# Kernel optimization log

Hardware: AMD Instinct MI355X
Metric: run time of the kernel (lower is better)

The kernel has to match this reference:

```python
import jax, jax.numpy as jnp
import numpy as np
from jax import lax

B, K, C, P = 16, 4096, 256, 1024
NSAMPLE = 16
RADIUS = 0.3
NUM_CLASS, NUMD = 18, 1
OUT_CH = 3 + NUMD + NUM_CLASS  # 22
EPS = 1e-5


def fps(xyz, npoint):
    # furthest point sampling; xyz (B,N,3) -> (B,npoint) int32
    b, n, _ = xyz.shape
    def body(carry, _):
        mind, last = carry
        lx = jnp.take_along_axis(xyz, last[:, None, None], axis=1)  # (B,1,3)
        d = jnp.sum((xyz - lx) ** 2, -1)
        mind = jnp.minimum(mind, d)
        nxt = jnp.argmax(mind, -1).astype(jnp.int32)
        return (mind, nxt), nxt
    i0 = jnp.zeros((b,), jnp.int32)
    _, rest = lax.scan(body, (jnp.full((b, n), 1e10, xyz.dtype), i0), None, length=npoint - 1)
    return jnp.concatenate([i0[None], rest], 0).T  # (B,npoint)


def ball_query(xyz, new_xyz, radius, nsample):
    # first `nsample` points (in index order) within radius; pad with first hit
    k = xyz.shape[1]
    d2 = jnp.sum((new_xyz[:, :, None, :] - xyz[:, None, :, :]) ** 2, -1)  # (B,P,K)
    keyi = jnp.where(d2 < radius * radius, jnp.arange(k, dtype=jnp.int32), k)
    idx = jnp.sort(keyi, axis=-1)[..., :nsample]  # (B,P,S)
    first = idx[..., :1]
    idx = jnp.where(idx >= k, first, idx)
    return jnp.clip(idx, 0, k - 1)


def bn(x, g, b, axes):
    # BatchNorm (training-mode batch statistics), channel on last axis
    m = jnp.mean(x, axes, keepdims=True)
    v = jnp.var(x, axes, keepdims=True)
    return (x - m) * lax.rsqrt(v + EPS) * g + b


def setup_inputs() -> dict:
    key = jax.random.key(0)
    ks = jax.random.split(key, 24)
    s = 0.02
    inp = {
        'xyz': jax.random.normal(ks[0], (B, K, 3), jnp.float32),
        'features': jax.random.normal(ks[1], (B, C, K), jnp.float32),
        # shared MLP (Conv2d 1x1, no bias, followed by BN2d)
        'mlp_w0': jax.random.normal(ks[2], (128, C + 3), jnp.float32) * s,
        'mlp_g0': jnp.ones((128,), jnp.float32), 'mlp_be0': jnp.zeros((128,), jnp.float32),
        'mlp_w1': jax.random.normal(ks[3], (128, 128), jnp.float32) * s,
        'mlp_g1': jnp.ones((128,), jnp.float32), 'mlp_be1': jnp.zeros((128,), jnp.float32),
        'mlp_w2': jax.random.normal(ks[4], (128, 128), jnp.float32) * s,
        'mlp_g2': jnp.ones((128,), jnp.float32), 'mlp_be2': jnp.zeros((128,), jnp.float32),
        # head: conv1d(128,128)+bn, conv1d(128,128)+bn, conv1d(128,22)
        'w1': jax.random.normal(ks[5], (128, 128), jnp.float32) * s, 'b1': jnp.zeros((128,), jnp.float32),
        'g1': jnp.ones((128,), jnp.float32), 'be1': jnp.zeros((128,), jnp.float32),
        'w2': jax.random.normal(ks[6], (128, 128), jnp.float32) * s, 'b2': jnp.zeros((128,), jnp.float32),
        'g2': jnp.ones((128,), jnp.float32), 'be2': jnp.zeros((128,), jnp.float32),
        'w3': jax.random.normal(ks[7], (OUT_CH, 128), jnp.float32) * s, 'b3': jnp.zeros((OUT_CH,), jnp.float32),
    }
    return inp


def reference(xyz, features, mlp_w0, mlp_g0, mlp_be0, mlp_w1, mlp_g1, mlp_be1,
              mlp_w2, mlp_g2, mlp_be2, w1, b1, g1, be1, w2, b2, g2, be2, w3, b3):
    # --- vote aggregation: FPS + ball query + grouped shared-MLP + max pool ---
    fps_idx = fps(xyz, P)                                   # (B,P)
    new_xyz = jax.vmap(lambda p, i: p[i])(xyz, fps_idx)      # (B,P,3)
    gidx = ball_query(lax.stop_gradient(xyz), lax.stop_gradient(new_xyz), RADIUS, NSAMPLE)
    gxyz = jax.vmap(lambda p, i: p[i])(xyz, gidx)            # (B,P,S,3)
    gxyz = (gxyz - new_xyz[:, :, None, :]) / RADIUS          # normalize_xyz
    feats_t = jnp.swapaxes(features, 1, 2)                   # (B,K,C)
    gfeat = jax.vmap(lambda f, i: f[i])(feats_t, gidx)       # (B,P,S,C)
    h = jnp.concatenate([gxyz, gfeat], -1)                   # (B,P,S,3+C) use_xyz
    for w, g, b in ((mlp_w0, mlp_g0, mlp_be0), (mlp_w1, mlp_g1, mlp_be1), (mlp_w2, mlp_g2, mlp_be2)):
        h = jax.nn.relu(bn(jnp.einsum('bpsc,oc->bpso', h, w), g, b, (0, 1, 2)))
    agg = jnp.max(h, axis=2)                                 # (B,P,128)
    # --- conv1d + BN + ReLU head ---
    n1 = jax.nn.relu(bn(jnp.einsum('bpc,oc->bpo', agg, w1) + b1, g1, be1, (0, 1)))
    n2 = jax.nn.relu(bn(jnp.einsum('bpc,oc->bpo', n1, w2) + b2, g2, be2, (0, 1)))
    net = jnp.einsum('bpc,oc->bpo', n2, w3) + b3             # (B,P,3+numd+num_class)
    # --- decode_scores (mode='') ---
    center = new_xyz + net[..., :3]
    return jnp.concatenate([center, net[..., 3:]], -1)        # (B,P,22)
```

## Files before the change

kernel.cpp:

```cpp
#include <hip/hip_runtime.h>
#include <math.h>

#define Bsz 16
#define Kpt 4096
#define Cft 256
#define Pnp 1024
#define Smp 16
#define OUTCH 22
#define M0 (Bsz * Pnp * Smp)
#define M1 (Bsz * Pnp)
#define NSLOT 32

#define OFF_FT      ((size_t)0)
#define OFF_YA      ((size_t)8388608)
#define OFF_M2      ((size_t)25165824)
#define OFF_YF1     ((size_t)27262976)
#define OFF_YF2     ((size_t)28311552)
#define OFF_W0T     ((size_t)30408704)
#define OFF_W1T     ((size_t)30425088)
#define OFF_W2T     ((size_t)30433280)
#define OFF_WF1T    ((size_t)30441472)
#define OFF_WF2T    ((size_t)30449664)
#define OFF_STATS   ((size_t)30457856)
#define OFF_GIDX    ((size_t)30498816)
#define OFF_NEWXYZ  ((size_t)30760960)

#define ST_STRIDE (NSLOT * 256)

typedef __attribute__((ext_vector_type(8))) short bf16x8;
typedef __attribute__((ext_vector_type(4))) float f32x4;

__device__ __forceinline__ unsigned short f2bf(float x) {
    union { float f; unsigned u; } v; v.f = x;
    unsigned r = v.u + 0x7fffu + ((v.u >> 16) & 1u);
    return (unsigned short)(r >> 16);
}
__device__ __forceinline__ float bf2f(unsigned short u) {
    union { unsigned u; float f; } v; v.u = ((unsigned)u) << 16; return v.f;
}

__device__ __forceinline__ void read_stats(const float* st, int tid, float& sm, float& sq) {
    sm = 0.f; sq = 0.f;
#pragma unroll
    for (int s = 0; s < NSLOT; ++s) {
        sm += st[s * 256 + tid];
        sq += st[s * 256 + 128 + tid];
    }
}

template <int CTRL>
__device__ __forceinline__ unsigned long long dpp_max_step(unsigned long long key) {
    int lo = (int)(unsigned)key, hi = (int)(key >> 32);
    int slo = __builtin_amdgcn_update_dpp(0, lo, CTRL, 0xf, 0xf, true);
    int shi = __builtin_amdgcn_update_dpp(0, hi, CTRL, 0xf, 0xf, true);
    unsigned long long other = ((unsigned long long)(unsigned)shi << 32) | (unsigned)slo;
    return other > key ? other : key;
}

__global__ __launch_bounds__(256) void fps_fused(const float* __restrict__ xyz, float* __restrict__ new_xyz,
                                                 const float* __restrict__ features, unsigned short* __restrict__ ft,
                                                 const float* __restrict__ w0, const float* __restrict__ w1m,
                                                 const float* __restrict__ w2m, const float* __restrict__ wf1,
                                                 const float* __restrict__ wf2,
                                                 unsigned short* __restrict__ W0T, unsigned short* __restrict__ W1T,
                                                 unsigned short* __restrict__ W2T, unsigned short* __restrict__ WF1T,
                                                 unsigned short* __restrict__ WF2T) {
    __shared__ float4 xyz_s[Kpt];
    __shared__ unsigned long long red[2][4];
    int bid = blockIdx.x, tid = threadIdx.x;

    if (bid < 16) {
        int b = bid, wid = tid >> 6, lane = tid & 63;
        for (int k = tid; k < Kpt; k += 256) {
            float x = xyz[(size_t)b * Kpt * 3 + k * 3 + 0];
            float y = xyz[(size_t)b * Kpt * 3 + k * 3 + 1];
            float z = xyz[(size_t)b * Kpt * 3 + k * 3 + 2];
            xyz_s[k] = make_float4(x, y, z, 0.f);
        }
        __syncthreads();
        float px[16], py[16], pz[16], mind[16];
#pragma unroll
        for (int j = 0; j < 16; ++j) {
            float4 p = xyz_s[tid + j * 256];
            px[j] = p.x; py[j] = p.y; pz[j] = p.z;
            mind[j] = 1e10f;
        }
        float lx = xyz_s[0].x, ly = xyz_s[0].y, lz = xyz_s[0].z;
        if (tid == 0) {
            new_xyz[(size_t)b * Pnp * 3 + 0] = lx;
            new_xyz[(size_t)b * Pnp * 3 + 1] = ly;
            new_xyz[(size_t)b * Pnp * 3 + 2] = lz;
        }
        for (int it = 1; it < Pnp; ++it) {
            float bestv = -1.0f;
            int bestk = 0;
#pragma unroll
            for (int j = 0; j < 16; ++j) {
                float dx = __fsub_rn(px[j], lx);
                float dy = __fsub_rn(py[j], ly);
                float dz = __fsub_rn(pz[j], lz);
                float d = __fadd_rn(__fadd_rn(__fmul_rn(dx, dx), __fmul_rn(dy, dy)), __fmul_rn(dz, dz));
                float m = fminf(mind[j], d);
                mind[j] = m;
                if (m > bestv) { bestv = m; bestk = tid + j * 256; }
            }
            unsigned long long key = ((unsigned long long)__float_as_uint(bestv) << 32) | (unsigned)(~bestk);
            key = dpp_max_step<0x111>(key);
            key = dpp_max_step<0x112>(key);
            key = dpp_max_step<0x114>(key);
            key = dpp_max_step<0x118>(key);
            key = dpp_max_step<0x142>(key);
            key = dpp_max_step<0x143>(key);
            if (lane == 63) red[it & 1][wid] = key;
            __syncthreads();
            unsigned long long gkey = red[it & 1][0];
#pragma unroll
            for (int w = 1; w < 4; ++w) {
                unsigned long long ok = red[it & 1][w];
                if (ok > gkey) gkey = ok;
            }
            int win = (int)(~(unsigned)gkey);
            float4 c = xyz_s[win];
            lx = c.x; ly = c.y; lz = c.z;
            if (tid == 0) {
                size_t bp = (size_t)b * Pnp + it;
                new_xyz[bp * 3 + 0] = c.x;
                new_xyz[bp * 3 + 1] = c.y;
                new_xyz[bp * 3 + 2] = c.z;
            }
        }
    } else if (bid < 16 + 1024) {
        float* tile = (float*)xyz_s;
        int tx = tid & 31, ty = tid >> 5;
        int t0 = (bid - 16) * 16;
        for (int tt = 0; tt < 16; ++tt) {
            int t = t0 + tt;
            int k0 = (t & 127) << 5;
            int c0 = ((t >> 7) & 7) << 5;
            int b2 = t >> 10;
            __syncthreads();
#pragma unroll
            for (int j = 0; j < 4; ++j)
                tile[(ty + j * 8) * 33 + tx] = features[((size_t)b2 * Cft + c0 + ty + j * 8) * Kpt + k0 + tx];
            __syncthreads();
#pragma unroll
            for (int j = 0; j < 4; ++j)
                ft[((size_t)b2 * Kpt + k0 + ty + j * 8) * Cft + c0 + tx] = f2bf(tile[tx * 33 + ty + j * 8]);
        }
    } else {
        int base = (bid - (16 + 1024)) * 6144;
#pragma unroll 1
        for (int i = 0; i < 24; ++i) {
            int e = base + i * 256 + tid;
            const float* src; unsigned short* dst; int eo, stride, off;
            if (e < 32768) { src = w0; dst = W0T; eo = e; stride = 259; off = 3; }
            else {
                int r = e - 32768; int which = r >> 14; eo = r & 16383; stride = 128; off = 0;
                src = (which == 0) ? w1m : (which == 1) ? w2m : (which == 2) ? wf1 : wf2;
                dst = (which == 0) ? W1T : (which == 1) ? W2T : (which == 2) ? WF1T : WF2T;
            }
            int j = eo & 7, np = (eo >> 3) & 15, q = (eo >> 7) & 3, S = (eo >> 9) & 7, c = eo >> 12;
            dst[eo] = f2bf(src[(size_t)(S * 16 + np) * stride + off + c * 32 + q * 8 + j]);
        }
    }
}

__global__ __launch_bounds__(256) void ballq_kernel(const float* __restrict__ xyz, const float* __restrict__ new_xyz,
                                                    int* __restrict__ gidx) {
    __shared__ float xyz_s[Kpt * 3];
    __shared__ int idxbuf[64][16];
    __shared__ int have_s[64];
    int bx = blockIdx.x;
    int b = bx >> 4, chunk = bx & 15;
    int tid = threadIdx.x, w = tid >> 6, lane = tid & 63;
    for (int e = tid; e < Kpt * 3; e += 256) xyz_s[e] = xyz[(size_t)b * Kpt * 3 + e];
    __syncthreads();
    const float R2 = (float)(0.3 * 0.3);
    unsigned long long lmask = (lane == 63) ? 0x7fffffffffffffffull : ((1ull << lane) - 1ull);
    for (int t = 0; t < 16; ++t) {
        int ql = w * 16 + t;
        size_t bp = (size_t)b * Pnp + chunk * 64 + ql;
        float nx = new_xyz[bp * 3 + 0], ny = new_xyz[bp * 3 + 1], nz = new_xyz[bp * 3 + 2];
        int have = 0;
        for (int r = 0; r < 64; ++r) {
            int k = r * 64 + lane;
            float dx = __fsub_rn(nx, xyz_s[k * 3 + 0]);
            float dy = __fsub_rn(ny, xyz_s[k * 3 + 1]);
            float dz = __fsub_rn(nz, xyz_s[k * 3 + 2]);
            float d2 = __fadd_rn(__fadd_rn(__fmul_rn(dx, dx), __fmul_rn(dy, dy)), __fmul_rn(dz, dz));
            bool inb = d2 < R2;
            unsigned long long mask = __ballot(inb);
            if (mask) {
                int rank = __popcll(mask & lmask);
                if (inb && (have + rank) < 16) idxbuf[ql][have + rank] = k;
                have += __popcll(mask);
                if (have >= 16) break;
            }
        }
        if (lane == 0) have_s[ql] = (have > 16) ? 16 : have;
    }
    __syncthreads();
    for (int e = tid; e < 1024; e += 256) {
        int ql = e >> 4, slot = e & 15;
        int h = have_s[ql];
        int v = (h == 0) ? (Kpt - 1) : ((slot < h) ? idxbuf[ql][slot] : idxbuf[ql][0]);
        size_t bp = (size_t)b * Pnp + chunk * 64 + ql;
        gidx[bp * 16 + slot] = v;
    }
}

__global__ __launch_bounds__(256) void gemm0_mfma(const unsigned short* __restrict__ ft, const unsigned short* __restrict__ Bsw,
                                                  const float* __restrict__ xyz, const float* __restrict__ new_xyz,
                                                  const int* __restrict__ gidx, const float* __restrict__ w0,
                                                  unsigned short* __restrict__ yout, float* __restrict__ statsOut) {
    __shared__ unsigned short Asw[128 * 256];
    __shared__ unsigned short Bs[256 * 128];
    __shared__ float4 gxyz_s[128];
    __shared__ float4 w03s[128];
    __shared__ int krow_s[128];
    __shared__ float ssum[128], ssq[128];
    int tid = threadIdx.x;
    int wave = tid >> 6, lane = tid & 63, q = lane >> 4, l = lane & 15;
    int wm = wave >> 1, wn = wave & 1;
    size_t r0 = (size_t)blockIdx.x * 128;
    int b = (int)(r0 >> 14);

    if (tid < 128) {
        ssum[tid] = 0.f; ssq[tid] = 0.f;
        size_t r = r0 + tid;
        int kg = gidx[r];
        krow_s[tid] = kg;
        size_t bp = r >> 4;
        float gx = (xyz[((size_t)b * Kpt + kg) * 3 + 0] - new_xyz[bp * 3 + 0]) / 0.3f;
        float gy = (xyz[((size_t)b * Kpt + kg) * 3 + 1] - new_xyz[bp * 3 + 1]) / 0.3f;
        float gz = (xyz[((size_t)b * Kpt + kg) * 3 + 2] - new_xyz[bp * 3 + 2]) / 0.3f;
        gxyz_s[tid] = make_float4(gx, gy, gz, 0.f);
    } else {
        int o = tid - 128;
        w03s[o] = make_float4(w0[(size_t)o * 259 + 0], w0[(size_t)o * 259 + 1], w0[(size_t)o * 259 + 2], 0.f);
    }
#pragma unroll
    for (int i = 0; i < 16; ++i) {
        int e = i * 256 + tid;
        *(int4*)&Bs[e * 8] = *(const int4*)&Bsw[e * 8];
    }
    __syncthreads();
#pragma unroll
    for (int i = 0; i < 16; ++i) {
        int idx = i * 4 + wave;
        int G = idx >> 3, c = idx & 7;
        int kg = krow_s[G * 16 + l];
        const unsigned short* src = ft + ((size_t)b * Kpt + kg) * 256 + c * 32 + q * 8;
        *(int4*)&Asw[(size_t)((c * 8 + G) * 64 + lane) * 8] = *(const int4*)src;
    }
    __syncthreads();

    f32x4 acc[4][4];
    f32x4 zz = {0.f, 0.f, 0.f, 0.f};
#pragma unroll
    for (int mi = 0; mi < 4; ++mi)
#pragma unroll
        for (int ni = 0; ni < 4; ++ni) acc[mi][ni] = zz;

    for (int c = 0; c < 8; ++c) {
        bf16x8 af[4], bfr[4];
#pragma unroll
        for (int mi = 0; mi < 4; ++mi)
            af[mi] = *(const bf16x8*)&Asw[(size_t)((c * 8 + wm * 4 + mi) * 64 + lane) * 8];
#pragma unroll
        for (int ni = 0; ni < 4; ++ni)
            bfr[ni] = *(const bf16x8*)&Bs[(size_t)((c * 8 + wn * 4 + ni) * 64 + lane) * 8];
#pragma unroll
        for (int mi = 0; mi < 4; ++mi)
#pragma unroll
            for (int ni = 0; ni < 4; ++ni)
                acc[mi][ni] = __builtin_amdgcn_mfma_f32_16x16x32_bf16(af[mi], bfr[ni], acc[mi][ni], 0, 0, 0);
    }
    float4 wv[4];
#pragma unroll
    for (int ni = 0; ni < 4; ++ni) wv[ni] = w03s[wn * 64 + ni * 16 + l];
    float psum[4] = {0.f, 0.f, 0.f, 0.f}, psq[4] = {0.f, 0.f, 0.f, 0.f};
#pragma unroll
    for (int mi = 0; mi < 4; ++mi) {
#pragma unroll
        for (int r = 0; r < 4; ++r) {
            int mloc = wm * 64 + mi * 16 + q * 4 + r;
            float4 g = gxyz_s[mloc];
            size_t rowg = r0 + mloc;
#pragma unroll
            for (int ni = 0; ni < 4; ++ni) {
                int colg = wn * 64 + ni * 16 + l;
                float val = acc[mi][ni][r] + g.x * wv[ni].x + g.y * wv[ni].y + g.z * wv[ni].z;
                psum[ni] += val; psq[ni] += val * val;
                yout[rowg * 128 + colg] = f2bf(val);
            }
        }
    }
#pragma unroll
    for (int ni = 0; ni < 4; ++ni) {
        float s = psum[ni], sq = psq[ni];
        s += __shfl_xor(s, 16); sq += __shfl_xor(sq, 16);
        s += __shfl_xor(s, 32); sq += __shfl_xor(sq, 32);
        if (q == 0) {
            int colg = wn * 64 + ni * 16 + l;
            atomicAdd(&ssum[colg], s);
            atomicAdd(&ssq[colg], sq);
        }
    }
    __syncthreads();
    if (tid < 128) {
        float* stSlot = statsOut + (blockIdx.x & (NSLOT - 1)) * 256;
        atomicAdd(&stSlot[tid], ssum[tid]);
        atomicAdd(&stSlot[128 + tid], ssq[tid]);
    }
}

__global__ __launch_bounds__(256) void gemm_mfma_bn(const unsigned short* __restrict__ A, const float* __restrict__ Af32,
                                                    const unsigned short* __restrict__ Bsw,
                                                    unsigned short* __restrict__ OutBf, float* __restrict__ OutF,
                                                    const float* __restrict__ statsIn, const float* __restrict__ gamma,
                                                    const float* __restrict__ beta, const float* __restrict__ bias,
                                                    float invN, float* __restrict__ statsOut) {
    __shared__ unsigned short Asw[128 * 128];
    __shared__ unsigned short Bs[128 * 128];
    __shared__ float scs[128], shs[128], ssum[128], ssq[128];
    int tid = threadIdx.x;
    int wave = tid >> 6, lane = tid & 63, q = lane >> 4, l = lane & 15;
    int wm = wave >> 1, wn = wave & 1;
    size_t r0 = (size_t)blockIdx.x * 128;
    bool hasT = (statsIn != nullptr);
    if (tid < 128) {
        ssum[tid] = 0.f; ssq[tid] = 0.f;
        if (hasT) {
            float sm, sq;
            read_stats(statsIn, tid, sm, sq);
            float m = sm * invN;
            float v = sq * invN - m * m;
            float sc = gamma[tid] / sqrtf(v + 1e-5f);
            scs[tid] = sc;
            shs[tid] = beta[tid] - m * sc;
        }
    }
#pragma unroll
    for (int i = 0; i < 8; ++i) {
        int e = i * 256 + tid;
        *(int4*)&Bs[e * 8] = *(const int4*)&Bsw[e * 8];
    }
    __syncthreads();
#pragma unroll
    for (int i = 0; i < 8; ++i) {
        int idx = i * 4 + wave;
        int G = idx >> 2, c = idx & 3;
        int cb = c * 32 + q * 8;
        int4 v;
        if (Af32) {
            const float* srcf = Af32 + (r0 + G * 16 + l) * 128 + cb;
            float4 v0 = *(const float4*)srcf;
            float4 v1 = *(const float4*)(srcf + 4);
            float vv[8] = {v0.x, v0.y, v0.z, v0.w, v1.x, v1.y, v1.z, v1.w};
            unsigned short* u = (unsigned short*)&v;
#pragma unroll
            for (int t = 0; t < 8; ++t) {
                float f = vv[t];
                if (hasT) f = fmaxf(0.f, f * scs[cb + t] + shs[cb + t]);
                u[t] = f2bf(f);
            }
        } else {
            const unsigned short* src = A + (r0 + G * 16 + l) * 128 + cb;
            v = *(const int4*)src;
            if (hasT) {
                unsigned short* u = (unsigned short*)&v;
#pragma unroll
                for (int t = 0; t < 8; ++t) {
                    float f = bf2f(u[t]);
                    u[t] = f2bf(fmaxf(0.f, f * scs[cb + t] + shs[cb + t]));
                }
            }
        }
        *(int4*)&Asw[(size_t)((c * 8 + G) * 64 + lane) * 8] = v;
    }
    __syncthreads();

    f32x4 acc[4][4];
    f32x4 zz = {0.f, 0.f, 0.f, 0.f};
#pragma unroll
    for (int mi = 0; mi < 4; ++mi)
#pragma unroll
        for (int ni = 0; ni < 4; ++ni) acc[mi][ni] = zz;

#pragma unroll
    for (int c = 0; c < 4; ++c) {
        bf16x8 af[4], bfr[4];
#pragma unroll
        for (int mi = 0; mi < 4; ++mi)
            af[mi] = *(const bf16x8*)&Asw[(size_t)((c * 8 + wm * 4 + mi) * 64 + lane) * 8];
#pragma unroll
        for (int ni = 0; ni < 4; ++ni)
            bfr[ni] = *(const bf16x8*)&Bs[(size_t)((c * 8 + wn * 4 + ni) * 64 + lane) * 8];
#pragma unroll
        for (int mi = 0; mi < 4; ++mi)
#pragma unroll
            for (int ni = 0; ni < 4; ++ni)
                acc[mi][ni] = __builtin_amdgcn_mfma_f32_16x16x32_bf16(af[mi], bfr[ni], acc[mi][ni], 0, 0, 0);
    }
    float psum[4] = {0.f, 0.f, 0.f, 0.f}, psq[4] = {0.f, 0.f, 0.f, 0.f};
#pragma unroll
    for (int mi = 0; mi < 4; ++mi) {
#pragma unroll
        for (int r = 0; r < 4; ++r) {
            size_t rowg = r0 + wm * 64 + mi * 16 + q * 4 + r;
#pragma unroll
            for (int ni = 0; ni < 4; ++ni) {
                int colg = wn * 64 + ni * 16 + l;
                float val = acc[mi][ni][r] + (bias ? bias[colg] : 0.f);
                psum[ni] += val; psq[ni] += val * val;
                if (OutBf) OutBf[rowg * 128 + colg] = f2bf(val);
                else OutF[rowg * 128 + colg] = val;
            }
        }
    }
#pragma unroll
    for (int ni = 0; ni < 4; ++ni) {
        float s = psum[ni], sq = psq[ni];
        s += __shfl_xor(s, 16); sq += __shfl_xor(sq, 16);
        s += __shfl_xor(s, 32); sq += __shfl_xor(sq, 32);
        if (q == 0) {
            int colg = wn * 64 + ni * 16 + l;
            atomicAdd(&ssum[colg], s);
            atomicAdd(&ssq[colg], sq);
        }
    }
    __syncthreads();
    if (tid < 128) {
        float* stSlot = statsOut + (blockIdx.x & (NSLOT - 1)) * 256;
        atomicAdd(&stSlot[tid], ssum[tid]);
        atomicAdd(&stSlot[128 + tid], ssq[tid]);
    }
}

__global__ __launch_bounds__(256) void gemm2_max(const unsigned short* __restrict__ A, const unsigned short* __restrict__ Bsw,
                                                 const float* __restrict__ statsIn, const float* __restrict__ gamma,
                                                 const float* __restrict__ beta, float invN,
                                                 float* __restrict__ m2, float* __restrict__ statsOut) {
    __shared__ unsigned short Asw[128 * 128];
    __shared__ unsigned short Bs[128 * 128];
    __shared__ float scs[128], shs[128], ssum[128], ssq[128];
    __shared__ float smax[8][128];
    int tid = threadIdx.x;
    int wave = tid >> 6, lane = tid & 63, q = lane >> 4, l = lane & 15;
    int wm = wave >> 1, wn = wave & 1;
    size_t r0 = (size_t)blockIdx.x * 128;
    if (tid < 128) {
        ssum[tid] = 0.f; ssq[tid] = 0.f;
        float sm, sq;
        read_stats(statsIn, tid, sm, sq);
        float m = sm * invN;
        float v = sq * invN - m * m;
        float sc = gamma[tid] / sqrtf(v + 1e-5f);
        scs[tid] = sc;
        shs[tid] = beta[tid] - m * sc;
    }
#pragma unroll
    for (int i = 0; i < 8; ++i) {
        int e = i * 256 + tid;
        *(int4*)&Bs[e * 8] = *(const int4*)&Bsw[e * 8];
    }
    __syncthreads();
#pragma unroll
    for (int i = 0; i < 8; ++i) {
        int idx = i * 4 + wave;
        int G = idx >> 2, c = idx & 3;
        const unsigned short* src = A + (r0 + G * 16 + l) * 128 + c * 32 + q * 8;
        int4 v = *(const int4*)src;
        unsigned short* u = (unsigned short*)&v;
        int cb = c * 32 + q * 8;
#pragma unroll
        for (int t = 0; t < 8; ++t) {
            float f = bf2f(u[t]);
            u[t] = f2bf(fmaxf(0.f, f * scs[cb + t] + shs[cb + t]));
        }
        *(int4*)&Asw[(size_t)((c * 8 + G) * 64 + lane) * 8] = v;
    }
    __syncthreads();

    f32x4 acc[4][4];
    f32x4 zz = {0.f, 0.f, 0.f, 0.f};
#pragma unroll
    for (int mi = 0; mi < 4; ++mi)
#pragma unroll
        for (int ni = 0; ni < 4; ++ni) acc[mi][ni] = zz;

#pragma unroll
    for (int c = 0; c < 4; ++c) {
        bf16x8 af[4], bfr[4];
#pragma unroll
        for (int mi = 0; mi < 4; ++mi)
            af[mi] = *(const bf16x8*)&Asw[(size_t)((c * 8 + wm * 4 + mi) * 64 + lane) * 8];
#pragma unroll
        for (int ni = 0; ni < 4; ++ni)
            bfr[ni] = *(const bf16x8*)&Bs[(size_t)((c * 8 + wn * 4 + ni) * 64 + lane) * 8];
#pragma unroll
        for (int mi = 0; mi < 4; ++mi)
#pragma unroll
            for (int ni = 0; ni < 4; ++ni)
                acc[mi][ni] = __builtin_amdgcn_mfma_f32_16x16x32_bf16(af[mi], bfr[ni], acc[mi][ni], 0, 0, 0);
    }
    float psum[4] = {0.f, 0.f, 0.f, 0.f}, psq[4] = {0.f, 0.f, 0.f, 0.f};
#pragma unroll
    for (int mi = 0; mi < 4; ++mi) {
#pragma unroll
        for (int ni = 0; ni < 4; ++ni) {
            float gm = -1e30f;
#pragma unroll
            for (int r = 0; r < 4; ++r) {
                float val = acc[mi][ni][r];
                psum[ni] += val; psq[ni] += val * val;
                gm = fmaxf(gm, val);
            }
            gm = fmaxf(gm, __shfl_xor(gm, 16));
            gm = fmaxf(gm, __shfl_xor(gm, 32));
            if (q == 0) smax[wm * 4 + mi][wn * 64 + ni * 16 + l] = gm;
        }
    }
#pragma unroll
    for (int ni = 0; ni < 4; ++ni) {
        float s = psum[ni], sq = psq[ni];
        s += __shfl_xor(s, 16); sq += __shfl_xor(sq, 16);
        s += __shfl_xor(s, 32); sq += __shfl_xor(sq, 32);
        if (q == 0) {
            int colg = wn * 64 + ni * 16 + l;
            atomicAdd(&ssum[colg], s);
            atomicAdd(&ssq[colg], sq);
        }
    }
    __syncthreads();
#pragma unroll
    for (int i = 0; i < 4; ++i) {
        int e = i * 256 + tid;
        int g = e >> 7, cc = e & 127;
        m2[((size_t)blockIdx.x * 8 + g) * 128 + cc] = smax[g][cc];
    }
    if (tid < 128) {
        float* stSlot = statsOut + (blockIdx.x & (NSLOT - 1)) * 256;
        atomicAdd(&stSlot[tid], ssum[tid]);
        atomicAdd(&stSlot[128 + tid], ssq[tid]);
    }
}

__global__ __launch_bounds__(256) void final_k(const float* __restrict__ yf, const float* __restrict__ st,
                                               const float* __restrict__ gamma, const float* __restrict__ beta,
                                               const float* __restrict__ w3, const float* __restrict__ b3,
                                               const float* __restrict__ new_xyz, float* __restrict__ out) {
    __shared__ float n2s[8][128];
    __shared__ float w3s[22 * 132];
    __shared__ float scf[128], shf[128];
    int tid = threadIdx.x;
    size_t r0 = (size_t)blockIdx.x * 8;
    if (tid < 128) {
        const float invN = 1.f / (float)M1;
        float sm, sq;
        read_stats(st, tid, sm, sq);
        float m = sm * invN;
        float v = sq * invN - m * m;
        float sc = gamma[tid] / sqrtf(v + 1e-5f);
        scf[tid] = sc;
        shf[tid] = beta[tid] - m * sc;
    }
    __syncthreads();
#pragma unroll
    for (int i = 0; i < 4; ++i) {
        int e = tid + i * 256;
        int rl = e >> 7, c = e & 127;
        float raw = yf[(r0 + rl) * 128 + c];
        n2s[rl][c] = fmaxf(0.f, raw * scf[c] + shf[c]);
    }
#pragma unroll
    for (int i = 0; i < 11; ++i) {
        int e = tid + i * 256;
        int o = e >> 7, c = e & 127;
        w3s[o * 132 + c] = w3[e];
    }
    __syncthreads();
    int rl = tid >> 5, o = tid & 31;
    if (o < OUTCH) {
        float dot = 0.f;
#pragma unroll 4
        for (int c = 0; c < 128; ++c) dot += n2s[rl][c] * w3s[o * 132 + c];
        float v = dot + b3[o];
        if (o < 3) v += new_xyz[(r0 + rl) * 3 + o];
        out[(r0 + rl) * OUTCH + o] = v;
    }
}

extern "C" void kernel_launch(void* const* d_in, const int* in_sizes, int n_in,
                              void* d_out, int out_size, void* d_ws, size_t ws_size,
                              hipStream_t stream) {
    (void)in_sizes; (void)n_in; (void)out_size; (void)ws_size;
    const float* xyz = (const float*)d_in[0];
    const float* features = (const float*)d_in[1];
    const float* w0 = (const float*)d_in[2];
    const float* g0 = (const float*)d_in[3];
    const float* be0 = (const float*)d_in[4];
    const float* w1m = (const float*)d_in[5];
    const float* g1m = (const float*)d_in[6];
    const float* be1m = (const float*)d_in[7];
    const float* w2m = (const float*)d_in[8];
    const float* g2m = (const float*)d_in[9];
    const float* be2m = (const float*)d_in[10];
    const float* wf1 = (const float*)d_in[11];
    const float* bf1 = (const float*)d_in[12];
    const float* gf1 = (const float*)d_in[13];
    const float* bef1 = (const float*)d_in[14];
    const float* wf2 = (const float*)d_in[15];
    const float* bf2 = (const float*)d_in[16];
    const float* gf2 = (const float*)d_in[17];
    const float* bef2 = (const float*)d_in[18];
    const float* w3 = (const float*)d_in[19];
    const float* b3 = (const float*)d_in[20];
    float* ws = (float*)d_ws;
    unsigned short* ft = (unsigned short*)(ws + OFF_FT);
    unsigned short* yA = (unsigned short*)(ws + OFF_YA);
    float* m2 = ws + OFF_M2;
    unsigned short* yF1 = (unsigned short*)(ws + OFF_YF1);
    float* yF2 = ws + OFF_YF2;
    unsigned short* W0T = (unsigned short*)(ws + OFF_W0T);
    unsigned short* W1T = (unsigned short*)(ws + OFF_W1T);
    unsigned short* W2T = (unsigned short*)(ws + OFF_W2T);
    unsigned short* WF1T = (unsigned short*)(ws + OFF_WF1T);
    unsigned short* WF2T = (unsigned short*)(ws + OFF_WF2T);
    float* st = ws + OFF_STATS;
    int* gidx = (int*)(ws + OFF_GIDX);
    float* nxyz = ws + OFF_NEWXYZ;

    hipMemsetAsync((void*)st, 0, 5 * ST_STRIDE * sizeof(float), stream);

    fps_fused<<<16 + 1024 + 16, 256, 0, stream>>>(xyz, nxyz, features, ft,
                                                  w0, w1m, w2m, wf1, wf2,
                                                  W0T, W1T, W2T, WF1T, WF2T);
    ballq_kernel<<<256, 256, 0, stream>>>(xyz, nxyz, gidx);

    gemm0_mfma<<<M0 / 128, 256, 0, stream>>>(ft, W0T, xyz, nxyz, gidx, w0, yA, st);
    gemm_mfma_bn<<<M0 / 128, 256, 0, stream>>>(yA, nullptr, W1T, yA, nullptr,
                                               st, g0, be0, nullptr, 1.f / (float)M0, st + ST_STRIDE);
    gemm2_max<<<M0 / 128, 256, 0, stream>>>(yA, W2T, st + ST_STRIDE, g1m, be1m, 1.f / (float)M0,
                                            m2, st + 2 * ST_STRIDE);
    gemm_mfma_bn<<<M1 / 128, 256, 0, stream>>>(nullptr, m2, WF1T, yF1, nullptr,
                                               st + 2 * ST_STRIDE, g2m, be2m, bf1, 1.f / (float)M0, st + 3 * ST_STRIDE);
    gemm_mfma_bn<<<M1 / 128, 256, 0, stream>>>(yF1, nullptr, WF2T, nullptr, yF2,
                                               st + 3 * ST_STRIDE, gf1, bef1, bf2, 1.f / (float)M1, st + 4 * ST_STRIDE);
    final_k<<<M1 / 8, 256, 0, stream>>>(yF2, st + 4 * ST_STRIDE, gf2, bef2, w3, b3, nxyz, (float*)d_out);
}
```

Before: 1.013 ms.

## Read GEMM weights directly from global memory and pad ball-query points to float4

```diff
diff --git a/kernel.cpp b/kernel.cpp
--- a/kernel.cpp
+++ b/kernel.cpp
@@ -167,13 +167,18 @@
 
 __global__ __launch_bounds__(256) void ballq_kernel(const float* __restrict__ xyz, const float* __restrict__ new_xyz,
                                                     int* __restrict__ gidx) {
-    __shared__ float xyz_s[Kpt * 3];
+    __shared__ float4 xyz_s[Kpt];
     __shared__ int idxbuf[64][16];
     __shared__ int have_s[64];
     int bx = blockIdx.x;
     int b = bx >> 4, chunk = bx & 15;
     int tid = threadIdx.x, w = tid >> 6, lane = tid & 63;
-    for (int e = tid; e < Kpt * 3; e += 256) xyz_s[e] = xyz[(size_t)b * Kpt * 3 + e];
+    for (int k = tid; k < Kpt; k += 256) {
+        float x = xyz[(size_t)b * Kpt * 3 + k * 3 + 0];
+        float y = xyz[(size_t)b * Kpt * 3 + k * 3 + 1];
+        float z = xyz[(size_t)b * Kpt * 3 + k * 3 + 2];
+        xyz_s[k] = make_float4(x, y, z, 0.f);
+    }
     __syncthreads();
     const float R2 = (float)(0.3 * 0.3);
     unsigned long long lmask = (lane == 63) ? 0x7fffffffffffffffull : ((1ull << lane) - 1ull);
@@ -182,20 +187,19 @@
         size_t bp = (size_t)b * Pnp + chunk * 64 + ql;
         float nx = new_xyz[bp * 3 + 0], ny = new_xyz[bp * 3 + 1], nz = new_xyz[bp * 3 + 2];
         int have = 0;
+#pragma unroll 4
         for (int r = 0; r < 64; ++r) {
             int k = r * 64 + lane;
-            float dx = __fsub_rn(nx, xyz_s[k * 3 + 0]);
-            float dy = __fsub_rn(ny, xyz_s[k * 3 + 1]);
-            float dz = __fsub_rn(nz, xyz_s[k * 3 + 2]);
+            float4 p = xyz_s[k];
+            float dx = __fsub_rn(nx, p.x);
+            float dy = __fsub_rn(ny, p.y);
+            float dz = __fsub_rn(nz, p.z);
             float d2 = __fadd_rn(__fadd_rn(__fmul_rn(dx, dx), __fmul_rn(dy, dy)), __fmul_rn(dz, dz));
             bool inb = d2 < R2;
             unsigned long long mask = __ballot(inb);
-            if (mask) {
-                int rank = __popcll(mask & lmask);
-                if (inb && (have + rank) < 16) idxbuf[ql][have + rank] = k;
-                have += __popcll(mask);
-                if (have >= 16) break;
-            }
+            int rank = __popcll(mask & lmask);
+            if (inb && (have + rank) < 16) idxbuf[ql][have + rank] = k;
+            have += __popcll(mask);
         }
         if (lane == 0) have_s[ql] = (have > 16) ? 16 : have;
     }
@@ -214,7 +218,6 @@
                                                   const int* __restrict__ gidx, const float* __restrict__ w0,
                                                   unsigned short* __restrict__ yout, float* __restrict__ statsOut) {
     __shared__ unsigned short Asw[128 * 256];
-    __shared__ unsigned short Bs[256 * 128];
     __shared__ float4 gxyz_s[128];
     __shared__ float4 w03s[128];
     __shared__ int krow_s[128];
@@ -239,11 +242,6 @@
         int o = tid - 128;
         w03s[o] = make_float4(w0[(size_t)o * 259 + 0], w0[(size_t)o * 259 + 1], w0[(size_t)o * 259 + 2], 0.f);
     }
-#pragma unroll
-    for (int i = 0; i < 16; ++i) {
-        int e = i * 256 + tid;
-        *(int4*)&Bs[e * 8] = *(const int4*)&Bsw[e * 8];
-    }
     __syncthreads();
 #pragma unroll
     for (int i = 0; i < 16; ++i) {
@@ -265,11 +263,11 @@
     for (int c = 0; c < 8; ++c) {
         bf16x8 af[4], bfr[4];
 #pragma unroll
+        for (int ni = 0; ni < 4; ++ni)
+            bfr[ni] = *(const bf16x8*)&Bsw[(size_t)((c * 8 + wn * 4 + ni) * 64 + lane) * 8];
+#pragma unroll
         for (int mi = 0; mi < 4; ++mi)
             af[mi] = *(const bf16x8*)&Asw[(size_t)((c * 8 + wm * 4 + mi) * 64 + lane) * 8];
-#pragma unroll
-        for (int ni = 0; ni < 4; ++ni)
-            bfr[ni] = *(const bf16x8*)&Bs[(size_t)((c * 8 + wn * 4 + ni) * 64 + lane) * 8];
 #pragma unroll
         for (int mi = 0; mi < 4; ++mi)
 #pragma unroll
@@ -322,7 +320,6 @@
                                                     const float* __restrict__ beta, const float* __restrict__ bias,
                                                     float invN, float* __restrict__ statsOut) {
     __shared__ unsigned short Asw[128 * 128];
-    __shared__ unsigned short Bs[128 * 128];
     __shared__ float scs[128], shs[128], ssum[128], ssq[128];
     int tid = threadIdx.x;
     int wave = tid >> 6, lane = tid & 63, q = lane >> 4, l = lane & 15;
@@ -341,11 +338,6 @@
             shs[tid] = beta[tid] - m * sc;
         }
     }
-#pragma unroll
-    for (int i = 0; i < 8; ++i) {
-        int e = i * 256 + tid;
-        *(int4*)&Bs[e * 8] = *(const int4*)&Bsw[e * 8];
-    }
     __syncthreads();
 #pragma unroll
     for (int i = 0; i < 8; ++i) {
@@ -392,11 +384,11 @@
     for (int c = 0; c < 4; ++c) {
         bf16x8 af[4], bfr[4];
 #pragma unroll
+        for (int ni = 0; ni < 4; ++ni)
+            bfr[ni] = *(const bf16x8*)&Bsw[(size_t)((c * 8 + wn * 4 + ni) * 64 + lane) * 8];
+#pragma unroll
         for (int mi = 0; mi < 4; ++mi)
             af[mi] = *(const bf16x8*)&Asw[(size_t)((c * 8 + wm * 4 + mi) * 64 + lane) * 8];
-#pragma unroll
-        for (int ni = 0; ni < 4; ++ni)
-            bfr[ni] = *(const bf16x8*)&Bs[(size_t)((c * 8 + wn * 4 + ni) * 64 + lane) * 8];
 #pragma unroll
         for (int mi = 0; mi < 4; ++mi)
 #pragma unroll
@@ -443,7 +435,6 @@
                                                  const float* __restrict__ beta, float invN,
                                                  float* __restrict__ m2, float* __restrict__ statsOut) {
     __shared__ unsigned short Asw[128 * 128];
-    __shared__ unsigned short Bs[128 * 128];
     __shared__ float scs[128], shs[128], ssum[128], ssq[128];
     __shared__ float smax[8][128];
     int tid = threadIdx.x;
@@ -460,11 +451,6 @@
         scs[tid] = sc;
         shs[tid] = beta[tid] - m * sc;
     }
-#pragma unroll
-    for (int i = 0; i < 8; ++i) {
-        int e = i * 256 + tid;
-        *(int4*)&Bs[e * 8] = *(const int4*)&Bsw[e * 8];
-    }
     __syncthreads();
 #pragma unroll
     for (int i = 0; i < 8; ++i) {
@@ -494,11 +480,11 @@
     for (int c = 0; c < 4; ++c) {
         bf16x8 af[4], bfr[4];
 #pragma unroll
+        for (int ni = 0; ni < 4; ++ni)
+            bfr[ni] = *(const bf16x8*)&Bsw[(size_t)((c * 8 + wn * 4 + ni) * 64 + lane) * 8];
+#pragma unroll
         for (int mi = 0; mi < 4; ++mi)
             af[mi] = *(const bf16x8*)&Asw[(size_t)((c * 8 + wm * 4 + mi) * 64 + lane) * 8];
-#pragma unroll
-        for (int ni = 0; ni < 4; ++ni)
-            bfr[ni] = *(const bf16x8*)&Bs[(size_t)((c * 8 + wn * 4 + ni) * 64 + lane) * 8];
 #pragma unroll
         for (int mi = 0; mi < 4; ++mi)
 #pragma unroll
```

New measurement: 955.4 us. 5.7% less time.
